# Performance work log

Measured on AMD Instinct MI355X. Metric: run time of the kernel, lower is better.

The kernel has to match this reference:

```python
import jax, jax.numpy as jnp
import numpy as np

N_NODES = 50000


def setup_inputs() -> dict:
    key = jax.random.key(0)
    k1, k2, k3, k4, k5 = jax.random.split(key, 5)
    x = jax.random.normal(k1, (N_NODES, 256), dtype=jnp.float32)
    edge_row = jax.random.randint(k2, (800000,), 0, N_NODES, dtype=jnp.int32)
    edge_col = jax.random.randint(k3, (800000,), 0, N_NODES, dtype=jnp.int32)
    edge_val = jax.random.uniform(k4, (800000,), dtype=jnp.float32)
    W = jax.random.normal(k5, (256, 256), dtype=jnp.float32) * 0.0625  # ~1/sqrt(256)
    b = jnp.zeros((256,), dtype=jnp.float32)
    return {"x": x, "edge_row": edge_row, "edge_col": edge_col,
            "edge_val": edge_val, "W": W, "b": b}


def reference(x, edge_row, edge_col, edge_val, W, b):
    # SpMM: agg[i] = sum_{e: row(e)=i} val(e) * x[col(e)]
    msgs = edge_val[:, None] * x[edge_col]                      # [E, F_in]
    agg = jax.ops.segment_sum(msgs, edge_row, num_segments=N_NODES)  # [N, F_in]
    # nn.Linear: agg @ W.T + b
    return jnp.einsum('nf,of->no', agg, W) + b
```

## Files before the change

kernel.cpp:

```cpp
#include <hip/hip_runtime.h>

typedef unsigned short u16;
typedef __attribute__((ext_vector_type(8))) short short8;
typedef __attribute__((ext_vector_type(4))) float f32x4;
typedef __attribute__((ext_vector_type(4))) u16 u16x4;

#define F 256

__device__ __forceinline__ u16 f2bf(float f) {
  unsigned u = __float_as_uint(f);
  unsigned r = u + 0x7fffu + ((u >> 16) & 1u);
  return (u16)(r >> 16);
}

__device__ __forceinline__ f32x4 bf4_to_f32(u16x4 u) {
  f32x4 x;
#pragma unroll
  for (int j = 0; j < 4; j++) x[j] = __uint_as_float((unsigned)u[j] << 16);
  return x;
}

__device__ __forceinline__ void gemm_body(const float* __restrict__ x,
                                          const float* __restrict__ Wm,
                                          u16* __restrict__ yb,
                                          int NT, int gidx, int stride) {
  int w = (int)(threadIdx.x >> 6);
  int lane = threadIdx.x & 63;
  int ln = lane & 15, q = lane >> 4;

  short8 Bf[4][8];
#pragma unroll
  for (int j = 0; j < 4; j++) {
#pragma unroll
    for (int t = 0; t < 8; t++) {
      const f32x4* wp = (const f32x4*)(Wm + (size_t)((4 * w + j) * 16 + ln) * F + t * 32 + q * 8);
      f32x4 wlo = wp[0], whi = wp[1];
      short8 bfrag;
#pragma unroll
      for (int i = 0; i < 4; i++) {
        bfrag[i]     = (short)f2bf(wlo[i]);
        bfrag[4 + i] = (short)f2bf(whi[i]);
      }
      Bf[j][t] = bfrag;
    }
  }

  for (int mt = gidx; mt < NT; mt += stride) {
    const float* arow = x + (size_t)(mt * 16 + ln) * F + q * 8;
    f32x4 acc[4];
#pragma unroll
    for (int j = 0; j < 4; j++) acc[j] = (f32x4){0.f, 0.f, 0.f, 0.f};

#pragma unroll
    for (int t = 0; t < 8; t++) {
      const f32x4* a4 = (const f32x4*)(arow + t * 32);
      f32x4 alo = a4[0], ahi = a4[1];
      short8 a;
#pragma unroll
      for (int j = 0; j < 4; j++) {
        a[j]     = (short)f2bf(alo[j]);
        a[4 + j] = (short)f2bf(ahi[j]);
      }
#pragma unroll
      for (int j = 0; j < 4; j++) {
        acc[j] = __builtin_amdgcn_mfma_f32_16x16x32_bf16(a, Bf[j][t], acc[j], 0, 0, 0);
      }
    }

    int m0 = mt * 16;
#pragma unroll
    for (int j = 0; j < 4; j++) {
#pragma unroll
      for (int r = 0; r < 4; r++) {
        yb[(size_t)(m0 + q * 4 + r) * F + (4 * w + j) * 16 + ln] = f2bf(acc[j][r]);
      }
    }
  }
}

#define NGEMM 512
#define NSCAT 3584
__global__ void __launch_bounds__(256, 1) gemmscat_k(const float* __restrict__ x,
                                                     const float* __restrict__ Wm,
                                                     u16* __restrict__ yb, int NT,
                                                     const int* __restrict__ erow,
                                                     const int* __restrict__ ecol,
                                                     const float* __restrict__ eval,
                                                     int* __restrict__ curp,
                                                     int2* __restrict__ epk,
                                                     int E, int CAP) {
  int bid = (int)blockIdx.x;
  if (bid < NGEMM) {
    gemm_body(x, Wm, yb, NT, bid, NGEMM);
  } else {
    int sid = bid - NGEMM;
    for (int e = sid * 256 + (int)threadIdx.x; e < E; e += NSCAT * 256) {
      int r = erow[e];
      int p = atomicAdd(&curp[r << 4], 1);
      if (p < CAP) epk[(size_t)r * CAP + p] = make_int2(ecol[e], __float_as_int(eval[e]));
    }
  }
}

__global__ void __launch_bounds__(256) gather_dir_k(const int* __restrict__ curp,
                                                    const int2* __restrict__ epk,
                                                    const u16* __restrict__ yb,
                                                    const float* __restrict__ bias,
                                                    float* __restrict__ out, int NN) {
  int wave = (int)((blockIdx.x * 256 + threadIdx.x) >> 6);
  int lane = threadIdx.x & 63;
  if (wave >= NN) return;
  int deg = curp[wave << 4];
  if (deg > 64) deg = 64;

  int2 m = epk[(size_t)wave * 64 + lane];
  int mc = m.x, mv = m.y;
  const u16* ybl = yb + lane * 4;

  f32x4 acc0 = ((const f32x4*)bias)[lane];
  f32x4 acc1 = (f32x4){0.f, 0.f, 0.f, 0.f};
  f32x4 acc2 = (f32x4){0.f, 0.f, 0.f, 0.f};
  f32x4 acc3 = (f32x4){0.f, 0.f, 0.f, 0.f};

  int k = 0;
  for (; k + 8 <= deg; k += 8) {
    int c0 = __shfl(mc, k + 0), c1 = __shfl(mc, k + 1);
    int c2 = __shfl(mc, k + 2), c3 = __shfl(mc, k + 3);
    int c4 = __shfl(mc, k + 4), c5 = __shfl(mc, k + 5);
    int c6 = __shfl(mc, k + 6), c7 = __shfl(mc, k + 7);
    u16x4 u0 = *(const u16x4*)(ybl + (size_t)c0 * F);
    u16x4 u1 = *(const u16x4*)(ybl + (size_t)c1 * F);
    u16x4 u2 = *(const u16x4*)(ybl + (size_t)c2 * F);
    u16x4 u3 = *(const u16x4*)(ybl + (size_t)c3 * F);
    u16x4 u4 = *(const u16x4*)(ybl + (size_t)c4 * F);
    u16x4 u5 = *(const u16x4*)(ybl + (size_t)c5 * F);
    u16x4 u6 = *(const u16x4*)(ybl + (size_t)c6 * F);
    u16x4 u7 = *(const u16x4*)(ybl + (size_t)c7 * F);
    float v0 = __int_as_float(__shfl(mv, k + 0)), v1 = __int_as_float(__shfl(mv, k + 1));
    float v2 = __int_as_float(__shfl(mv, k + 2)), v3 = __int_as_float(__shfl(mv, k + 3));
    float v4 = __int_as_float(__shfl(mv, k + 4)), v5 = __int_as_float(__shfl(mv, k + 5));
    float v6 = __int_as_float(__shfl(mv, k + 6)), v7 = __int_as_float(__shfl(mv, k + 7));
    acc0 += v0 * bf4_to_f32(u0);
    acc1 += v1 * bf4_to_f32(u1);
    acc2 += v2 * bf4_to_f32(u2);
    acc3 += v3 * bf4_to_f32(u3);
    acc0 += v4 * bf4_to_f32(u4);
    acc1 += v5 * bf4_to_f32(u5);
    acc2 += v6 * bf4_to_f32(u6);
    acc3 += v7 * bf4_to_f32(u7);
  }
  for (; k < deg; k++) {
    int c = __shfl(mc, k);
    float v = __int_as_float(__shfl(mv, k));
    u16x4 u = *(const u16x4*)(ybl + (size_t)c * F);
    acc0 += v * bf4_to_f32(u);
  }
  acc0 += acc1;
  acc2 += acc3;
  acc0 += acc2;
  ((f32x4*)out)[(size_t)wave * 64 + lane] = acc0;
}


__global__ void hist_k(const int* __restrict__ erow, int* __restrict__ off, int E) {
  int e = blockIdx.x * 256 + threadIdx.x;
  if (e < E) atomicAdd(&off[erow[e] + 1], 1);
}

__global__ void scanA_k(int* __restrict__ a, int* __restrict__ blks, int n) {
  __shared__ int s[256];
  int t = threadIdx.x;
  int i = blockIdx.x * 256 + t;
  s[t] = (i < n) ? a[i] : 0;
  __syncthreads();
  for (int d = 1; d < 256; d <<= 1) {
    int v = (t >= d) ? s[t - d] : 0;
    __syncthreads();
    s[t] += v;
    __syncthreads();
  }
  if (i < n) a[i] = s[t];
  if (t == 255) blks[blockIdx.x] = s[255];
}

__global__ void scanB_k(int* __restrict__ a, const int* __restrict__ blks,
                        int* __restrict__ cur, int n, int nn, int nb) {
  __shared__ int s[256];
  int t = threadIdx.x;
  s[t] = (t < nb) ? blks[t] : 0;
  __syncthreads();
  for (int d = 1; d < 256; d <<= 1) {
    int v = (t >= d) ? s[t - d] : 0;
    __syncthreads();
    s[t] += v;
    __syncthreads();
  }
  int prefix = (blockIdx.x == 0) ? 0 : s[blockIdx.x - 1];
  int i = blockIdx.x * 256 + t;
  if (i < n) {
    int v = a[i] + prefix;
    a[i] = v;
    if (i < nn) cur[i] = v;
  }
}

__global__ void scatter_csr_k(const int* __restrict__ erow, const int* __restrict__ ecol,
                              const float* __restrict__ eval, int* __restrict__ cur,
                              int2* __restrict__ epk, int E) {
  int e = blockIdx.x * 256 + threadIdx.x;
  if (e < E) {
    int r = erow[e];
    int p = atomicAdd(&cur[r], 1);
    epk[p] = make_int2(ecol[e], __float_as_int(eval[e]));
  }
}

__global__ void __launch_bounds__(256) gather_csr_k(const int* __restrict__ off,
                                                    const int2* __restrict__ epk,
                                                    const u16* __restrict__ yb,
                                                    const float* __restrict__ bias,
                                                    float* __restrict__ out, int NN) {
  int wave = (int)((blockIdx.x * 256 + threadIdx.x) >> 6);
  int lane = threadIdx.x & 63;
  if (wave >= NN) return;
  int s = off[wave], e = off[wave + 1];

  f32x4 acc0 = ((const f32x4*)bias)[lane];
  f32x4 acc1 = (f32x4){0.f, 0.f, 0.f, 0.f};
  f32x4 acc2 = (f32x4){0.f, 0.f, 0.f, 0.f};
  f32x4 acc3 = (f32x4){0.f, 0.f, 0.f, 0.f};

  int k = s;
  for (; k + 4 <= e; k += 4) {
    int2 p0 = epk[k], p1 = epk[k + 1], p2 = epk[k + 2], p3 = epk[k + 3];
    u16x4 u0 = *(const u16x4*)(yb + (size_t)p0.x * F + lane * 4);
    u16x4 u1 = *(const u16x4*)(yb + (size_t)p1.x * F + lane * 4);
    u16x4 u2 = *(const u16x4*)(yb + (size_t)p2.x * F + lane * 4);
    u16x4 u3 = *(const u16x4*)(yb + (size_t)p3.x * F + lane * 4);
    acc0 += __int_as_float(p0.y) * bf4_to_f32(u0);
    acc1 += __int_as_float(p1.y) * bf4_to_f32(u1);
    acc2 += __int_as_float(p2.y) * bf4_to_f32(u2);
    acc3 += __int_as_float(p3.y) * bf4_to_f32(u3);
  }
  for (; k < e; k++) {
    int2 p = epk[k];
    u16x4 u = *(const u16x4*)(yb + (size_t)p.x * F + lane * 4);
    acc0 += __int_as_float(p.y) * bf4_to_f32(u);
  }
  acc0 += acc1;
  acc2 += acc3;
  acc0 += acc2;
  ((f32x4*)out)[(size_t)wave * 64 + lane] = acc0;
}

__global__ void __launch_bounds__(256, 1) gemm_only_k(const float* __restrict__ x,
                                                      const float* __restrict__ Wm,
                                                      u16* __restrict__ yb, int NT, int stride) {
  gemm_body(x, Wm, yb, NT, blockIdx.x, stride);
}

extern "C" void kernel_launch(void* const* d_in, const int* in_sizes, int n_in,
                              void* d_out, int out_size, void* d_ws, size_t ws_size,
                              hipStream_t stream) {
  const float* x    = (const float*)d_in[0];
  const int*   erow = (const int*)d_in[1];
  const int*   ecol = (const int*)d_in[2];
  const float* eval = (const float*)d_in[3];
  const float* Wm   = (const float*)d_in[4];
  const float* bias = (const float*)d_in[5];
  float* out = (float*)d_out;

  int NN = in_sizes[0] / F;
  int E  = in_sizes[1];

  char* base = (char*)d_ws;
  size_t o = 0;
  auto carve = [&](size_t bytes) {
    void* p = base + o;
    o += (bytes + 255) & ~(size_t)255;
    return p;
  };
  u16* yb   = (u16*)carve((size_t)NN * F * 2);
  int* curp = (int*)carve((size_t)NN * 64);

  size_t avail = (ws_size > o) ? (ws_size - o) : 0;
  size_t capmax = avail / ((size_t)NN * 8);
  int CAP = 64;

  int NT = (NN + 15) / 16;

  if (capmax >= 64) {
    int2* epk = (int2*)carve((size_t)NN * CAP * 8);
    hipMemsetAsync(curp, 0, (size_t)NN * 64, stream);
    gemmscat_k<<<NGEMM + NSCAT, 256, 0, stream>>>(x, Wm, yb, NT, erow, ecol, eval, curp, epk, E, CAP);
    gather_dir_k<<<(NN + 3) / 4, 256, 0, stream>>>(curp, epk, yb, bias, out, NN);
  } else {
    int*  cur  = curp;
    int*  off  = (int*)carve((size_t)(NN + 1) * 4);
    int*  blks = (int*)carve(256 * 4);
    int2* epk  = (int2*)carve((size_t)E * 8);
    int nOff = NN + 1;
    int nbOff = (nOff + 255) / 256;
    int nbE = (E + 255) / 256;
    hipMemsetAsync(off, 0, (size_t)nOff * 4, stream);
    hist_k<<<nbE, 256, 0, stream>>>(erow, off, E);
    scanA_k<<<nbOff, 256, 0, stream>>>(off, blks, nOff);
    scanB_k<<<nbOff, 256, 0, stream>>>(off, blks, cur, nOff, NN, nbOff);
    scatter_csr_k<<<nbE, 256, 0, stream>>>(erow, ecol, eval, cur, epk, E);
    gemm_only_k<<<512, 256, 0, stream>>>(x, Wm, yb, NT, 512);
    gather_csr_k<<<(NN + 3) / 4, 256, 0, stream>>>(off, epk, yb, bias, out, NN);
  }
}
```

Baseline: 253.3 us.

## Split x bf16 conversion into separate pass fused with edge scatter, then bf16 GEMM

Replaces the fused GEMM+scatter kernel with a kernel that converts x to bf16 while other blocks scatter edges into per-row buckets. A separate GEMM kernel then reads the bf16 x with one-step software prefetch of A fragments. The aim is to halve the GEMM's activation read traffic and remove conversion ALU work from the MFMA loop. The cost is an extra full pass writing and rereading a bf16 copy of x, one more launch, and the loss of overlap between the GEMM and the scatter.

```diff
diff --git a/kernel.cpp b/kernel.cpp
--- a/kernel.cpp
+++ b/kernel.cpp
@@ -2,10 +2,12 @@
 
 typedef unsigned short u16;
 typedef __attribute__((ext_vector_type(8))) short short8;
+typedef __attribute__((ext_vector_type(8))) u16 u16x8;
 typedef __attribute__((ext_vector_type(4))) float f32x4;
 typedef __attribute__((ext_vector_type(4))) u16 u16x4;
 
 #define F 256
+#define NCV 2048
 
 __device__ __forceinline__ u16 f2bf(float f) {
   unsigned u = __float_as_uint(f);
@@ -20,10 +22,39 @@
   return x;
 }
 
-__device__ __forceinline__ void gemm_body(const float* __restrict__ x,
-                                          const float* __restrict__ Wm,
-                                          u16* __restrict__ yb,
-                                          int NT, int gidx, int stride) {
+__global__ void __launch_bounds__(256) convscat_k(const float* __restrict__ x,
+                                                  u16* __restrict__ xb, int nchunks,
+                                                  const int* __restrict__ erow,
+                                                  const int* __restrict__ ecol,
+                                                  const float* __restrict__ eval,
+                                                  int* __restrict__ curp,
+                                                  int2* __restrict__ epk, int E, int CAP) {
+  int bid = (int)blockIdx.x;
+  if (bid < NCV) {
+    for (int i = bid * 256 + (int)threadIdx.x; i < nchunks; i += NCV * 256) {
+      const f32x4* p = (const f32x4*)x + 2 * (size_t)i;
+      f32x4 lo = p[0], hi = p[1];
+      u16x8 v;
+#pragma unroll
+      for (int j = 0; j < 4; j++) {
+        v[j]     = f2bf(lo[j]);
+        v[4 + j] = f2bf(hi[j]);
+      }
+      ((u16x8*)xb)[i] = v;
+    }
+  } else {
+    int e = (bid - NCV) * 256 + (int)threadIdx.x;
+    if (e < E) {
+      int r = erow[e];
+      int p = atomicAdd(&curp[r << 4], 1);
+      if (p < CAP) epk[(size_t)r * CAP + p] = make_int2(ecol[e], __float_as_int(eval[e]));
+    }
+  }
+}
+
+__global__ void __launch_bounds__(256, 1) gemmb_k(const u16* __restrict__ xb,
+                                                  const float* __restrict__ Wm,
+                                                  u16* __restrict__ yb, int NT, int stride) {
   int w = (int)(threadIdx.x >> 6);
   int lane = threadIdx.x & 63;
   int ln = lane & 15, q = lane >> 4;
@@ -45,26 +76,22 @@
     }
   }
 
-  for (int mt = gidx; mt < NT; mt += stride) {
-    const float* arow = x + (size_t)(mt * 16 + ln) * F + q * 8;
+  for (int mt = (int)blockIdx.x; mt < NT; mt += stride) {
+    const u16* arow = xb + (size_t)(mt * 16 + ln) * F + q * 8;
     f32x4 acc[4];
 #pragma unroll
     for (int j = 0; j < 4; j++) acc[j] = (f32x4){0.f, 0.f, 0.f, 0.f};
 
+    short8 a_cur = *(const short8*)arow;
 #pragma unroll
     for (int t = 0; t < 8; t++) {
-      const f32x4* a4 = (const f32x4*)(arow + t * 32);
-      f32x4 alo = a4[0], ahi = a4[1];
-      short8 a;
+      short8 a_nxt;
+      if (t < 7) a_nxt = *(const short8*)(arow + (t + 1) * 32);
 #pragma unroll
       for (int j = 0; j < 4; j++) {
-        a[j]     = (short)f2bf(alo[j]);
-        a[4 + j] = (short)f2bf(ahi[j]);
-      }
-#pragma unroll
-      for (int j = 0; j < 4; j++) {
-        acc[j] = __builtin_amdgcn_mfma_f32_16x16x32_bf16(a, Bf[j][t], acc[j], 0, 0, 0);
-      }
+        acc[j] = __builtin_amdgcn_mfma_f32_16x16x32_bf16(a_cur, Bf[j][t], acc[j], 0, 0, 0);
+      }
+      a_cur = a_nxt;
     }
 
     int m0 = mt * 16;
@@ -78,27 +105,16 @@
   }
 }
 
-#define NGEMM 512
-#define NSCAT 3584
-__global__ void __launch_bounds__(256, 1) gemmscat_k(const float* __restrict__ x,
-                                                     const float* __restrict__ Wm,
-                                                     u16* __restrict__ yb, int NT,
-                                                     const int* __restrict__ erow,
-                                                     const int* __restrict__ ecol,
-                                                     const float* __restrict__ eval,
-                                                     int* __restrict__ curp,
-                                                     int2* __restrict__ epk,
-                                                     int E, int CAP) {
-  int bid = (int)blockIdx.x;
-  if (bid < NGEMM) {
-    gemm_body(x, Wm, yb, NT, bid, NGEMM);
-  } else {
-    int sid = bid - NGEMM;
-    for (int e = sid * 256 + (int)threadIdx.x; e < E; e += NSCAT * 256) {
-      int r = erow[e];
-      int p = atomicAdd(&curp[r << 4], 1);
-      if (p < CAP) epk[(size_t)r * CAP + p] = make_int2(ecol[e], __float_as_int(eval[e]));
-    }
+__global__ void __launch_bounds__(256) scatter_k(const int* __restrict__ erow,
+                                                 const int* __restrict__ ecol,
+                                                 const float* __restrict__ eval,
+                                                 int* __restrict__ curp,
+                                                 int2* __restrict__ epk, int E, int CAP) {
+  int e = blockIdx.x * 256 + (int)threadIdx.x;
+  if (e < E) {
+    int r = erow[e];
+    int p = atomicAdd(&curp[r << 4], 1);
+    if (p < CAP) epk[(size_t)r * CAP + p] = make_int2(ecol[e], __float_as_int(eval[e]));
   }
 }
 
@@ -161,6 +177,70 @@
   ((f32x4*)out)[(size_t)wave * 64 + lane] = acc0;
 }
 
+__device__ __forceinline__ void gemm_body(const float* __restrict__ x,
+                                          const float* __restrict__ Wm,
+                                          u16* __restrict__ yb,
+                                          int NT, int gidx, int stride) {
+  int w = (int)(threadIdx.x >> 6);
+  int lane = threadIdx.x & 63;
+  int ln = lane & 15, q = lane >> 4;
+
+  short8 Bf[4][8];
+#pragma unroll
+  for (int j = 0; j < 4; j++) {
+#pragma unroll
+    for (int t = 0; t < 8; t++) {
+      const f32x4* wp = (const f32x4*)(Wm + (size_t)((4 * w + j) * 16 + ln) * F + t * 32 + q * 8);
+      f32x4 wlo = wp[0], whi = wp[1];
+      short8 bfrag;
+#pragma unroll
+      for (int i = 0; i < 4; i++) {
+        bfrag[i]     = (short)f2bf(wlo[i]);
+        bfrag[4 + i] = (short)f2bf(whi[i]);
+      }
+      Bf[j][t] = bfrag;
+    }
+  }
+
+  for (int mt = gidx; mt < NT; mt += stride) {
+    const float* arow = x + (size_t)(mt * 16 + ln) * F + q * 8;
+    f32x4 acc[4];
+#pragma unroll
+    for (int j = 0; j < 4; j++) acc[j] = (f32x4){0.f, 0.f, 0.f, 0.f};
+
+#pragma unroll
+    for (int t = 0; t < 8; t++) {
+      const f32x4* a4 = (const f32x4*)(arow + t * 32);
+      f32x4 alo = a4[0], ahi = a4[1];
+      short8 a;
+#pragma unroll
+      for (int j = 0; j < 4; j++) {
+        a[j]     = (short)f2bf(alo[j]);
+        a[4 + j] = (short)f2bf(ahi[j]);
+      }
+#pragma unroll
+      for (int j = 0; j < 4; j++) {
+        acc[j] = __builtin_amdgcn_mfma_f32_16x16x32_bf16(a, Bf[j][t], acc[j], 0, 0, 0);
+      }
+    }
+
+    int m0 = mt * 16;
+#pragma unroll
+    for (int j = 0; j < 4; j++) {
+#pragma unroll
+      for (int r = 0; r < 4; r++) {
+        yb[(size_t)(m0 + q * 4 + r) * F + (4 * w + j) * 16 + ln] = f2bf(acc[j][r]);
+      }
+    }
+  }
+}
+
+__global__ void __launch_bounds__(256, 1) gemm_only_k(const float* __restrict__ x,
+                                                      const float* __restrict__ Wm,
+                                                      u16* __restrict__ yb, int NT, int stride) {
+  gemm_body(x, Wm, yb, NT, blockIdx.x, stride);
+}
+
 
 __global__ void hist_k(const int* __restrict__ erow, int* __restrict__ off, int E) {
   int e = blockIdx.x * 256 + threadIdx.x;
@@ -253,12 +333,6 @@
   ((f32x4*)out)[(size_t)wave * 64 + lane] = acc0;
 }
 
-__global__ void __launch_bounds__(256, 1) gemm_only_k(const float* __restrict__ x,
-                                                      const float* __restrict__ Wm,
-                                                      u16* __restrict__ yb, int NT, int stride) {
-  gemm_body(x, Wm, yb, NT, blockIdx.x, stride);
-}
-
 extern "C" void kernel_launch(void* const* d_in, const int* in_sizes, int n_in,
                               void* d_out, int out_size, void* d_ws, size_t ws_size,
                               hipStream_t stream) {
@@ -291,8 +365,18 @@
 
   if (capmax >= 64) {
     int2* epk = (int2*)carve((size_t)NN * CAP * 8);
+    int nbE = (E + 255) / 256;
+    bool has_xb = (ws_size >= o + (size_t)NN * F * 2 + 256);
     hipMemsetAsync(curp, 0, (size_t)NN * 64, stream);
-    gemmscat_k<<<NGEMM + NSCAT, 256, 0, stream>>>(x, Wm, yb, NT, erow, ecol, eval, curp, epk, E, CAP);
+    if (has_xb) {
+      u16* xb = (u16*)carve((size_t)NN * F * 2);
+      int nchunks = NN * F / 8;
+      convscat_k<<<NCV + nbE, 256, 0, stream>>>(x, xb, nchunks, erow, ecol, eval, curp, epk, E, CAP);
+      gemmb_k<<<512, 256, 0, stream>>>(xb, Wm, yb, NT, 512);
+    } else {
+      scatter_k<<<nbE, 256, 0, stream>>>(erow, ecol, eval, curp, epk, E, CAP);
+      gemm_only_k<<<512, 256, 0, stream>>>(x, Wm, yb, NT, 512);
+    }
     gather_dir_k<<<(NN + 3) / 4, 256, 0, stream>>>(curp, epk, yb, bias, out, NN);
   } else {
     int*  cur  = curp;
```

After: 243.5 us. -3.9%, faster.
